# Performance work log

Hardware: AMD Instinct MI355X
Metric: run time of the kernel (lower is better)

Reference implementation:

```python
import jax, jax.numpy as jnp
import numpy as np

R_CUTOFF = 5.0
BASIS = 8
NMAX = 8
NSPECIES = 3
EMBED = 16


def _chebyshev_basis(r, r_cutoff, basis_size):
    fc = jnp.where(r < r_cutoff, 0.5 * jnp.cos(jnp.pi * r / r_cutoff) + 0.5, 0.0)
    x = 2.0 * (r / r_cutoff) ** 2 - 1.0
    polys = [jnp.ones_like(x), x]
    for n in range(2, basis_size):
        polys.append(2.0 * x * polys[-1] - polys[-2])
    basis = jnp.stack(polys[:basis_size], axis=-1)  # [E, basis]
    return 0.5 * (basis + 1.0) * fc[:, None]


def setup_inputs() -> dict:
    key = jax.random.key(0)
    ks = jax.random.split(key, 12)
    N, K = 20000, 32
    E = N * K
    positions = jax.random.normal(ks[0], (N, 3), dtype=jnp.float32)
    species = jax.random.randint(ks[1], (N,), 0, NSPECIES, dtype=jnp.int32)
    magmoms = jax.random.normal(ks[2], (N, 3), dtype=jnp.float32)
    # i-major edge list: exactly K edges per atom, grouped by center atom.
    i_idx = jnp.repeat(jnp.arange(N, dtype=jnp.int32), K)
    j_idx = jax.random.randint(ks[3], (E,), 0, N, dtype=jnp.int32)
    edge_index = jnp.stack([i_idx, j_idx], axis=0)
    shifts = jnp.zeros((E, 3), dtype=jnp.float32)
    rb_coefficients = 0.1 * jax.random.normal(ks[4], (NSPECIES * NSPECIES, NMAX, BASIS), dtype=jnp.float32)
    species_embedding = 0.1 * jax.random.normal(ks[5], (NSPECIES, EMBED), dtype=jnp.float32)
    struct_dim = NMAX + NMAX * (NMAX + 1)  # 80
    mag_dim = 3 + 7 * NMAX + 3 * NMAX * NMAX  # 251
    return {
        'positions': positions, 'species': species, 'magmoms': magmoms,
        'edge_index': edge_index, 'shifts': shifts,
        'rb_coefficients': rb_coefficients, 'species_embedding': species_embedding,
        'struct_shift': jnp.zeros(struct_dim, jnp.float32),
        'struct_scale': jnp.ones(struct_dim, jnp.float32),
        'mag_shift': jnp.zeros(mag_dim, jnp.float32),
        'mag_scale': jnp.ones(mag_dim, jnp.float32),
        'atomic_energy_shift': 0.1 * jax.random.normal(ks[6], (NSPECIES,), dtype=jnp.float32),
        'w_struct': 0.05 * jax.random.normal(ks[7], (EMBED + struct_dim,), dtype=jnp.float32),
        'b_struct': 0.05 * jax.random.normal(ks[8], (1,), dtype=jnp.float32),
        'w_mag': 0.05 * jax.random.normal(ks[9], (EMBED + mag_dim,), dtype=jnp.float32),
        'b_mag': 0.05 * jax.random.normal(ks[10], (1,), dtype=jnp.float32),
    }


def _forward(positions, magmoms, shifts, rb_coefficients, species_embedding,
             struct_shift, struct_scale, mag_shift, mag_scale, atomic_energy_shift,
             w_struct, b_struct, w_mag, b_mag, species, edge_index):
    N = positions.shape[0]
    E = edge_index.shape[1]
    K = E // N  # regular neighbor count (edge list is i-major)
    i_idx, j_idx = edge_index[0], edge_index[1]
    r_ij = positions[j_idx] - positions[i_idx] + shifts          # [E,3]
    dist = jnp.linalg.norm(r_ij, axis=-1)                        # [E]
    f_k = _chebyshev_basis(dist, R_CUTOFF, BASIS)                # [E,basis]
    pair_idx = species[i_idx] * NSPECIES + species[j_idx]
    phi = jnp.einsum('enk,ek->en', rb_coefficients[pair_idx], f_k)  # [E,n]
    seg = lambda x: jax.ops.segment_sum(x, i_idx, num_segments=N)
    d = jnp.maximum(dist, 1e-8)[:, None]
    r_hat = r_ij / d
    # --- structural descriptors ---
    d_radial = seg(phi)                                          # [N,n]
    P = seg(phi[:, :, None] * r_hat[:, None, :])                 # [N,n,3]
    PP = jnp.einsum('ina,ima->inm', P, P)
    tu = np.triu_indices(NMAX)
    d_ang_l1 = PP[:, tu[0], tu[1]]
    eye3 = jnp.eye(3, dtype=r_ij.dtype)
    traceless = r_hat[:, :, None] * r_hat[:, None, :] - eye3 / 3.0  # [E,3,3]
    Q = seg(phi[:, :, None, None] * traceless[:, None, :, :])       # [N,n,3,3]
    Qf = Q.reshape(N, NMAX, 9)
    QQ = jnp.einsum('ina,ima->inm', Qf, Qf)
    d_ang_l2 = QQ[:, tu[0], tu[1]]
    desc_struct = jnp.concatenate([d_radial, d_ang_l1, d_ang_l2], axis=-1)
    # --- magnetic descriptors ---
    u = jnp.sum(magmoms * magmoms, axis=-1)                      # [N]
    m_norm = jnp.linalg.norm(magmoms, axis=-1, keepdims=True)
    m_dir = jnp.where(m_norm > 1e-8, magmoms / jnp.maximum(m_norm, 1e-8), 0.0)
    M = seg(phi[:, :, None] * m_dir[j_idx][:, None, :])          # [N,n,3]
    # A_{nm}(i) = sum_{a<b within atom i's edge block} phi_n(a) phi_m(b) (r_a x r_b)
    phi_g = phi.reshape(N, K, NMAX)
    r_g = r_ij.reshape(N, K, 3)
    cross = jnp.cross(r_g[:, :, None, :], r_g[:, None, :, :])    # [N,K,K,3]
    mask = jnp.triu(jnp.ones((K, K), dtype=phi.dtype), k=1)
    tmp = jnp.einsum('iabd,ab,ibm->iamd', cross, mask, phi_g)    # [N,K,3,n]
    A = jnp.einsum('ian,iamd->inmd', phi_g, tmp)                 # [N,n,n,3]
    d_amp = jnp.stack([u, u ** 2, u ** 3], axis=-1)
    d_iso = jnp.sum(m_dir[:, None, :] * M, axis=-1)              # [N,n]
    Qm = jnp.einsum('anij,aj->ani', Q, m_dir)
    d_sia = jnp.sum(m_dir[:, None, :] * Qm, axis=-1)
    mQ = jnp.einsum('ai,amij->amj', m_dir, Q)
    d_sae = jnp.einsum('amj,anj->amn', mQ, M).reshape(N, -1)
    m_cross_M = jnp.cross(jnp.broadcast_to(m_dir[:, None, :], M.shape), M)
    d_dmi = jnp.einsum('inmd,imd->inm', A, m_cross_M).reshape(N, -1)
    u_col = u[:, None]
    d_amp_mix = jnp.concatenate([u_col * d_iso, u_col * d_sia, u_col * d_dmi], axis=-1)
    u_j = u[j_idx]
    d_nbr_amp = seg(phi * u_j[:, None])
    W = seg(phi[:, :, None] * (u_j[:, None] * m_dir[j_idx])[:, None, :])
    d_nbr_amp_ex = jnp.sum(m_dir[:, None, :] * W, axis=-1)
    d_nbr_amp_ex_mix = u_col * d_nbr_amp_ex
    desc_mag = jnp.concatenate([d_amp, d_iso, d_sia, d_sae, d_dmi, d_amp_mix,
                                d_nbr_amp, d_nbr_amp_ex, d_nbr_amp_ex_mix], axis=-1)
    # --- scaling + linear readout heads + per-species shift ---
    ds = (desc_struct - struct_shift) / struct_scale
    dm = (desc_mag - mag_shift) / mag_scale
    emb = species_embedding[species]
    e_struct = jnp.concatenate([emb, ds], axis=-1) @ w_struct + b_struct[0]
    e_mag = jnp.concatenate([emb, dm], axis=-1) @ w_mag + b_mag[0]
    return e_struct + e_mag + atomic_energy_shift[species]        # [N]


def reference(positions, species, magmoms, edge_index, shifts, rb_coefficients,
              species_embedding, struct_shift, struct_scale, mag_shift, mag_scale,
              atomic_energy_shift, w_struct, b_struct, w_mag, b_mag):
    return _forward(positions, magmoms, shifts, rb_coefficients, species_embedding,
                    struct_shift, struct_scale, mag_shift, mag_scale, atomic_energy_shift,
                    w_struct, b_struct, w_mag, b_mag, species, edge_index)
```

## Files before the change

kernel.cpp:

```cpp
#include <hip/hip_runtime.h>

#define NSPEC  3
#define EMBEDD 16
#define KMAX   32
#define RCUT   5.0f
#define PADR   36

__constant__ int TUN[36] = {0,0,0,0,0,0,0,0, 1,1,1,1,1,1,1, 2,2,2,2,2,2, 3,3,3,3,3, 4,4,4,4, 5,5,5, 6,6, 7};
__constant__ int TUM[36] = {0,1,2,3,4,5,6,7, 1,2,3,4,5,6,7, 2,3,4,5,6,7, 3,4,5,6,7, 4,5,6,7, 5,6,7, 6,7, 7};


struct __align__(16) AtomLds {
    float phiT[8 * PADR];
    float tT[8 * PADR];
    float rhx[KMAX], rhy[KMAX], rhz[KMAX];
    float mdx[KMAX], mdy[KMAX], mdz[KMAX];
    float uj[KMAX];
    float P[24], Q[48], M[24], W[24], mQ[24];
};

__global__ __launch_bounds__(256)
void magpot_setup(const float* __restrict__ sshift, const float* __restrict__ sscale,
                  const float* __restrict__ mshift, const float* __restrict__ mscale,
                  const float* __restrict__ wstruct, const float* __restrict__ bstruct,
                  const float* __restrict__ wmag, const float* __restrict__ bmag,
                  float* __restrict__ ws)
{
    __shared__ float red[4];
    const int t = threadIdx.x;
    float c = 0.0f;
    for (int idx = t; idx < 80; idx += 256) {
        const float w = wstruct[16 + idx] / sscale[idx];
        ws[idx] = w;
        c += w * sshift[idx];
    }
    for (int idx = t; idx < 251; idx += 256) {
        const float w = wmag[16 + idx] / mscale[idx];
        ws[80 + idx] = w;
        c += w * mshift[idx];
    }
    if (t < EMBEDD) ws[332 + t] = wstruct[t] + wmag[t];
    #pragma unroll
    for (int d = 1; d <= 32; d <<= 1) c += __shfl_xor(c, d, 64);
    if ((t & 63) == 0) red[t >> 6] = c;
    __syncthreads();
    if (t == 0) ws[331] = bstruct[0] + bmag[0] - (red[0] + red[1] + red[2] + red[3]);
}

__global__ __launch_bounds__(256, 5)
void magpot_main(const float* __restrict__ pos,
                 const int*   __restrict__ species,
                 const float* __restrict__ mag,
                 const int*   __restrict__ eidx,
                 const float* __restrict__ shifts,
                 const float* __restrict__ rb,
                 const float* __restrict__ semb,
                 const float* __restrict__ aes,
                 const float* __restrict__ ws,
                 float* __restrict__ out,
                 int N, int E, int K)
{
    __shared__ AtomLds lds[8];

    const int lane64 = threadIdx.x & 63;
    const int wv     = threadIdx.x >> 6;
    const int h      = lane64 >> 5;
    const int s      = lane64 & 31;
    const int i      = blockIdx.x * 8 + wv * 2 + h;
    const bool valid = (i < N);
    const int isafe  = valid ? i : 0;
    AtomLds& L = lds[wv * 2 + h];

    const float* wm = ws + 80;

    const float pix = pos[3*isafe+0], piy = pos[3*isafe+1], piz = pos[3*isafe+2];
    const int   spi = species[isafe];
    const float mgx = mag[3*isafe+0], mgy = mag[3*isafe+1], mgz = mag[3*isafe+2];
    const float u_i = mgx*mgx + mgy*mgy + mgz*mgz;
    const float mn_i = sqrtf(u_i);
    const float mi_inv = (mn_i > 1e-8f) ? (1.0f / mn_i) : 0.0f;
    const float mix = mgx*mi_inv, miy = mgy*mi_inv, miz = mgz*mi_inv;

    float phi[8];
    float rx = 0.0f, ry = 0.0f, rz = 0.0f;
    #pragma unroll
    for (int n = 0; n < 8; ++n) phi[n] = 0.0f;

    if (s < K) {
        const int e = isafe * K + s;
        const int j = eidx[E + e];
        rx = pos[3*j+0] - pix + shifts[3*e+0];
        ry = pos[3*j+1] - piy + shifts[3*e+1];
        rz = pos[3*j+2] - piz + shifts[3*e+2];
        const float dist = sqrtf(rx*rx + ry*ry + rz*rz);
        const float fc = (dist < RCUT)
            ? (0.5f * cosf(3.14159265358979323846f * dist * (1.0f/RCUT)) + 0.5f)
            : 0.0f;
        const float xr = dist * (1.0f/RCUT);
        const float x  = 2.0f * xr * xr - 1.0f;
        float f[8];
        {
            float Tm2 = 1.0f, Tm1 = x;
            f[0] = 0.5f * (Tm2 + 1.0f) * fc;
            f[1] = 0.5f * (Tm1 + 1.0f) * fc;
            #pragma unroll
            for (int k = 2; k < 8; ++k) {
                const float T = 2.0f * x * Tm1 - Tm2;
                Tm2 = Tm1; Tm1 = T;
                f[k] = 0.5f * (T + 1.0f) * fc;
            }
        }
        const int spj = species[j];
        const float4* rb4 = (const float4*)(rb + (spi * NSPEC + spj) * 64);
        #pragma unroll
        for (int n = 0; n < 8; ++n) {
            const float4 r0 = rb4[n*2+0];
            const float4 r1 = rb4[n*2+1];
            const float ph = r0.x*f[0] + r0.y*f[1] + r0.z*f[2] + r0.w*f[3]
                           + r1.x*f[4] + r1.y*f[5] + r1.z*f[6] + r1.w*f[7];
            phi[n] = ph;
            L.phiT[n*PADR + s] = ph;
        }
        const float dinv = 1.0f / fmaxf(dist, 1e-8f);
        L.rhx[s] = rx * dinv;
        L.rhy[s] = ry * dinv;
        L.rhz[s] = rz * dinv;
        const float mjx = mag[3*j+0], mjy = mag[3*j+1], mjz = mag[3*j+2];
        const float uj = mjx*mjx + mjy*mjy + mjz*mjz;
        const float mnj = sqrtf(uj);
        const float mjinv = (mnj > 1e-8f) ? (1.0f / mnj) : 0.0f;
        L.mdx[s] = mjx * mjinv;
        L.mdy[s] = mjy * mjinv;
        L.mdz[s] = mjz * mjinv;
        L.uj[s] = uj;
    } else {
        #pragma unroll
        for (int n = 0; n < 8; ++n) L.phiT[n*PADR + s] = 0.0f;
        L.rhx[s] = 0.0f; L.rhy[s] = 0.0f; L.rhz[s] = 0.0f;
        L.mdx[s] = 0.0f; L.mdy[s] = 0.0f; L.mdz[s] = 0.0f;
        L.uj[s] = 0.0f;
    }
    __syncthreads();

    float p = 0.0f;

    {
        const int k4 = s >> 3;
        const int n  = s & 7;
        const float4* phR = (const float4*)&L.phiT[n*PADR + k4*8];
        const float4* hxR = (const float4*)&L.rhx[k4*8];
        const float4* hyR = (const float4*)&L.rhy[k4*8];
        const float4* hzR = (const float4*)&L.rhz[k4*8];
        const float4* dxR = (const float4*)&L.mdx[k4*8];
        const float4* dyR = (const float4*)&L.mdy[k4*8];
        const float4* dzR = (const float4*)&L.mdz[k4*8];
        const float4* ujR = (const float4*)&L.uj[k4*8];

        float a_dr = 0.0f;
        float aP0 = 0.0f, aP1 = 0.0f, aP2 = 0.0f;
        float aQ0 = 0.0f, aQ1 = 0.0f, aQ2 = 0.0f, aQ3 = 0.0f, aQ4 = 0.0f, aQ5 = 0.0f;
        float aM0 = 0.0f, aM1 = 0.0f, aM2 = 0.0f;
        float a_nb = 0.0f;
        float aW0 = 0.0f, aW1 = 0.0f, aW2 = 0.0f;

        auto acc = [&](float ph, float hx, float hy, float hz,
                       float dx, float dy, float dz, float uj) {
            a_dr += ph;
            aP0 += ph*hx; aP1 += ph*hy; aP2 += ph*hz;
            aQ0 += ph*(hx*hx - (1.0f/3.0f));
            aQ1 += ph*(hx*hy);
            aQ2 += ph*(hx*hz);
            aQ3 += ph*(hy*hy - (1.0f/3.0f));
            aQ4 += ph*(hy*hz);
            aQ5 += ph*(hz*hz - (1.0f/3.0f));
            aM0 += ph*dx; aM1 += ph*dy; aM2 += ph*dz;
            const float pu = ph*uj;
            a_nb += pu;
            aW0 += pu*dx; aW1 += pu*dy; aW2 += pu*dz;
        };
        #pragma unroll
        for (int q = 0; q < 2; ++q) {
            const float4 ph4 = phR[q], hx4 = hxR[q], hy4 = hyR[q], hz4 = hzR[q];
            const float4 dx4 = dxR[q], dy4 = dyR[q], dz4 = dzR[q], uj4 = ujR[q];
            acc(ph4.x, hx4.x, hy4.x, hz4.x, dx4.x, dy4.x, dz4.x, uj4.x);
            acc(ph4.y, hx4.y, hy4.y, hz4.y, dx4.y, dy4.y, dz4.y, uj4.y);
            acc(ph4.z, hx4.z, hy4.z, hz4.z, dx4.z, dy4.z, dz4.z, uj4.z);
            acc(ph4.w, hx4.w, hy4.w, hz4.w, dx4.w, dy4.w, dz4.w, uj4.w);
        }
        #pragma unroll
        for (int d = 8; d <= 16; d <<= 1) {
            a_dr += __shfl_xor(a_dr, d, 64);
            aP0 += __shfl_xor(aP0, d, 64); aP1 += __shfl_xor(aP1, d, 64); aP2 += __shfl_xor(aP2, d, 64);
            aQ0 += __shfl_xor(aQ0, d, 64); aQ1 += __shfl_xor(aQ1, d, 64); aQ2 += __shfl_xor(aQ2, d, 64);
            aQ3 += __shfl_xor(aQ3, d, 64); aQ4 += __shfl_xor(aQ4, d, 64); aQ5 += __shfl_xor(aQ5, d, 64);
            aM0 += __shfl_xor(aM0, d, 64); aM1 += __shfl_xor(aM1, d, 64); aM2 += __shfl_xor(aM2, d, 64);
            a_nb += __shfl_xor(a_nb, d, 64);
            aW0 += __shfl_xor(aW0, d, 64); aW1 += __shfl_xor(aW1, d, 64); aW2 += __shfl_xor(aW2, d, 64);
        }
        if (k4 == 0) {
            L.P[n*3+0] = aP0; L.P[n*3+1] = aP1; L.P[n*3+2] = aP2;
            L.Q[n*6+0] = aQ0; L.Q[n*6+1] = aQ1; L.Q[n*6+2] = aQ2;
            L.Q[n*6+3] = aQ3; L.Q[n*6+4] = aQ4; L.Q[n*6+5] = aQ5;
            L.M[n*3+0] = aM0; L.M[n*3+1] = aM1; L.M[n*3+2] = aM2;
            L.W[n*3+0] = aW0; L.W[n*3+1] = aW1; L.W[n*3+2] = aW2;
            p += a_dr * ws[n];
            p += a_nb * wm[227 + n];
        }
        if (s == 8) {
            const float u2 = u_i * u_i;
            p += u_i * wm[0] + u2 * wm[1] + u2 * u_i * wm[2];
        }
        if (s < EMBEDD)
            p += semb[spi * EMBEDD + s] * ws[332 + s];
    }
    __syncthreads();

    {
        float S[8][3];
        #pragma unroll
        for (int m = 0; m < 8; ++m) {
            S[m][0] = phi[m] * rx;
            S[m][1] = phi[m] * ry;
            S[m][2] = phi[m] * rz;
        }
        #pragma unroll
        for (int d = 1; d <= 16; d <<= 1) {
            const bool ok = (s + d) < 32;
            #pragma unroll
            for (int m = 0; m < 8; ++m) {
                const float v0 = __shfl_down(S[m][0], d, 64);
                const float v1 = __shfl_down(S[m][1], d, 64);
                const float v2 = __shfl_down(S[m][2], d, 64);
                S[m][0] += ok ? v0 : 0.0f;
                S[m][1] += ok ? v1 : 0.0f;
                S[m][2] += ok ? v2 : 0.0f;
            }
        }
        #pragma unroll
        for (int m = 0; m < 8; ++m) {
            const float Sx = S[m][0] - phi[m]*rx;
            const float Sy = S[m][1] - phi[m]*ry;
            const float Sz = S[m][2] - phi[m]*rz;
            const float Mx = L.M[m*3+0], My = L.M[m*3+1], Mz = L.M[m*3+2];
            const float wx = miy*Mz - miz*My;
            const float wy = miz*Mx - mix*Mz;
            const float wz = mix*My - miy*Mx;
            const float cx = ry*Sz - rz*Sy;
            const float cy = rz*Sx - rx*Sz;
            const float cz = rx*Sy - ry*Sx;
            L.tT[m*PADR + s] = cx*wx + cy*wy + cz*wz;
        }
    }
    __syncthreads();

    {
        const int n  = s >> 2;
        const int mb = (s & 3) << 1;
        const float4* phR = (const float4*)&L.phiT[n*PADR];
        const float4* t0R = (const float4*)&L.tT[mb*PADR];
        const float4* t1R = (const float4*)&L.tT[(mb+1)*PADR];
        float d0 = 0.0f, d1 = 0.0f;
        #pragma unroll
        for (int q = 0; q < 8; ++q) {
            const float4 pv = phR[q];
            const float4 t0 = t0R[q];
            const float4 t1 = t1R[q];
            d0 += pv.x*t0.x + pv.y*t0.y + pv.z*t0.z + pv.w*t0.w;
            d1 += pv.x*t1.x + pv.y*t1.y + pv.z*t1.z + pv.w*t1.w;
        }
        const int i0 = n*8 + mb;
        p += d0 * wm[83 + i0]     + (u_i * d0) * wm[163 + i0];
        p += d1 * wm[83 + i0 + 1] + (u_i * d1) * wm[163 + i0 + 1];
    }

    if (s < 8) {
        const int n = s;
        const float Mx = L.M[n*3+0], My = L.M[n*3+1], Mz = L.M[n*3+2];
        const float diso = mix*Mx + miy*My + miz*Mz;
        const float q0 = L.Q[n*6+0], q1 = L.Q[n*6+1], q2 = L.Q[n*6+2];
        const float q3 = L.Q[n*6+3], q4 = L.Q[n*6+4], q5 = L.Q[n*6+5];
        const float dsia = q0*mix*mix + q3*miy*miy + q5*miz*miz
                         + 2.0f*(q1*mix*miy + q2*mix*miz + q4*miy*miz);
        L.mQ[n*3+0] = q0*mix + q1*miy + q2*miz;
        L.mQ[n*3+1] = q1*mix + q3*miy + q4*miz;
        L.mQ[n*3+2] = q2*mix + q4*miy + q5*miz;
        const float wx = L.W[n*3+0], wy = L.W[n*3+1], wz = L.W[n*3+2];
        const float dnex = mix*wx + miy*wy + miz*wz;
        p += diso * wm[3 + n]  + dsia * wm[11 + n]  + dnex * wm[235 + n]
           + u_i * (diso * wm[147 + n] + dsia * wm[155 + n] + dnex * wm[243 + n]);
    }
    __syncthreads();

    {
        #pragma unroll
        for (int t2 = 0; t2 < 2; ++t2) {
            const int idx = s + t2*32;
            const int m4 = idx >> 3, n4 = idx & 7;
            const float sae = L.mQ[m4*3+0]*L.M[n4*3+0]
                            + L.mQ[m4*3+1]*L.M[n4*3+1]
                            + L.mQ[m4*3+2]*L.M[n4*3+2];
            p += sae * wm[19 + idx];
        }
        #pragma unroll
        for (int t2 = 0; t2 < 2; ++t2) {
            const int idx = s + t2*32;
            if (idx < 36) {
                const int a = TUN[idx], b = TUM[idx];
                const float pp = L.P[a*3+0]*L.P[b*3+0] + L.P[a*3+1]*L.P[b*3+1] + L.P[a*3+2]*L.P[b*3+2];
                const float qq = L.Q[a*6+0]*L.Q[b*6+0] + L.Q[a*6+3]*L.Q[b*6+3] + L.Q[a*6+5]*L.Q[b*6+5]
                       + 2.0f*(L.Q[a*6+1]*L.Q[b*6+1] + L.Q[a*6+2]*L.Q[b*6+2] + L.Q[a*6+4]*L.Q[b*6+4]);
                p += pp * ws[8 + idx] + qq * ws[44 + idx];
            }
        }
    }

    #pragma unroll
    for (int d = 1; d <= 16; d <<= 1) p += __shfl_xor(p, d, 64);
    if (s == 0 && valid)
        out[i] = p + ws[331] + aes[spi];
}

extern "C" void kernel_launch(void* const* d_in, const int* in_sizes, int n_in,
                              void* d_out, int out_size, void* d_ws, size_t ws_size,
                              hipStream_t stream) {
    const float* pos     = (const float*)d_in[0];
    const int*   spc     = (const int*)  d_in[1];
    const float* mg      = (const float*)d_in[2];
    const int*   eidx    = (const int*)  d_in[3];
    const float* shf     = (const float*)d_in[4];
    const float* rb      = (const float*)d_in[5];
    const float* semb    = (const float*)d_in[6];
    const float* sshift  = (const float*)d_in[7];
    const float* sscale  = (const float*)d_in[8];
    const float* mshift  = (const float*)d_in[9];
    const float* mscale  = (const float*)d_in[10];
    const float* aes     = (const float*)d_in[11];
    const float* wstruct = (const float*)d_in[12];
    const float* bstruct = (const float*)d_in[13];
    const float* wmag    = (const float*)d_in[14];
    const float* bmag    = (const float*)d_in[15];
    float* out = (float*)d_out;
    float* ws  = (float*)d_ws;

    const int N = in_sizes[1];
    const int E = in_sizes[3] / 2;
    const int K = E / N;

    hipLaunchKernelGGL(magpot_setup, dim3(1), dim3(256), 0, stream,
                       sshift, sscale, mshift, mscale, wstruct, bstruct, wmag, bmag, ws);
    hipLaunchKernelGGL(magpot_main, dim3((N + 7) / 8), dim3(256), 0, stream,
                       pos, spc, mg, eidx, shf, rb, semb, aes, ws, out, N, E, K);
}
```

Before: 133.1 us.

## Replace shuffle-based scans and reductions with DPP and swizzle cross-lane ops

The lane-to-edge mapping is reversed (edge = 31 - lane) so that an inclusive prefix sum built from DPP row_shr and row_bcast yields the suffix sums the exclusive-scan step needs. This replaces the 24-value shfl_down scan that went through LDS. The k-reductions and the final per-atom reduction also move from __shfl_xor to DPP row_shr/row_bcast plus ds_swizzle. cosf is swapped for the hardware cos builtin, and the occupancy hint in launch bounds is dropped. The risks are DPP bound_ctrl/row_mask correctness across the 32-lane half-waves and the lower precision of the hardware cosine.

```diff
diff --git a/kernel.cpp b/kernel.cpp
--- a/kernel.cpp
+++ b/kernel.cpp
@@ -9,6 +9,36 @@
 __constant__ int TUN[36] = {0,0,0,0,0,0,0,0, 1,1,1,1,1,1,1, 2,2,2,2,2,2, 3,3,3,3,3, 4,4,4,4, 5,5,5, 6,6, 7};
 __constant__ int TUM[36] = {0,1,2,3,4,5,6,7, 1,2,3,4,5,6,7, 2,3,4,5,6,7, 3,4,5,6,7, 4,5,6,7, 5,6,7, 6,7, 7};
 
+
+template<int CTRL, int RMASK, bool BC>
+__device__ __forceinline__ float dpp_mov0(float x) {
+    return __int_as_float(__builtin_amdgcn_update_dpp(
+        0, __float_as_int(x), CTRL, RMASK, 0xF, BC));
+}
+__device__ __forceinline__ float prefix32(float x) {
+    x += dpp_mov0<0x111, 0xF, true >(x);
+    x += dpp_mov0<0x112, 0xF, true >(x);
+    x += dpp_mov0<0x114, 0xF, true >(x);
+    x += dpp_mov0<0x118, 0xF, true >(x);
+    x += dpp_mov0<0x142, 0xA, false>(x);
+    return x;
+}
+__device__ __forceinline__ float swz_xor16(float x) {
+    return __int_as_float(__builtin_amdgcn_ds_swizzle(__float_as_int(x), 0x401F));
+}
+__device__ __forceinline__ float red_k4(float x) {
+    x += dpp_mov0<0x128, 0xF, true>(x);
+    x += swz_xor16(x);
+    return x;
+}
+__device__ __forceinline__ float red32(float x) {
+    x += dpp_mov0<0x121, 0xF, true>(x);
+    x += dpp_mov0<0x122, 0xF, true>(x);
+    x += dpp_mov0<0x124, 0xF, true>(x);
+    x += dpp_mov0<0x128, 0xF, true>(x);
+    x += swz_xor16(x);
+    return x;
+}
 
 struct __align__(16) AtomLds {
     float phiT[8 * PADR];
@@ -47,7 +77,7 @@
     if (t == 0) ws[331] = bstruct[0] + bmag[0] - (red[0] + red[1] + red[2] + red[3]);
 }
 
-__global__ __launch_bounds__(256, 5)
+__global__ __launch_bounds__(256)
 void magpot_main(const float* __restrict__ pos,
                  const int*   __restrict__ species,
                  const float* __restrict__ mag,
@@ -66,6 +96,7 @@
     const int wv     = threadIdx.x >> 6;
     const int h      = lane64 >> 5;
     const int s      = lane64 & 31;
+    const int ea     = 31 - s;
     const int i      = blockIdx.x * 8 + wv * 2 + h;
     const bool valid = (i < N);
     const int isafe  = valid ? i : 0;
@@ -86,15 +117,15 @@
     #pragma unroll
     for (int n = 0; n < 8; ++n) phi[n] = 0.0f;
 
-    if (s < K) {
-        const int e = isafe * K + s;
+    if (ea < K) {
+        const int e = isafe * K + ea;
         const int j = eidx[E + e];
         rx = pos[3*j+0] - pix + shifts[3*e+0];
         ry = pos[3*j+1] - piy + shifts[3*e+1];
         rz = pos[3*j+2] - piz + shifts[3*e+2];
         const float dist = sqrtf(rx*rx + ry*ry + rz*rz);
         const float fc = (dist < RCUT)
-            ? (0.5f * cosf(3.14159265358979323846f * dist * (1.0f/RCUT)) + 0.5f)
+            ? (0.5f * __builtin_amdgcn_cosf(dist * 0.1f) + 0.5f)
             : 0.0f;
         const float xr = dist * (1.0f/RCUT);
         const float x  = 2.0f * xr * xr - 1.0f;
@@ -119,26 +150,26 @@
             const float ph = r0.x*f[0] + r0.y*f[1] + r0.z*f[2] + r0.w*f[3]
                            + r1.x*f[4] + r1.y*f[5] + r1.z*f[6] + r1.w*f[7];
             phi[n] = ph;
-            L.phiT[n*PADR + s] = ph;
+            L.phiT[n*PADR + ea] = ph;
         }
         const float dinv = 1.0f / fmaxf(dist, 1e-8f);
-        L.rhx[s] = rx * dinv;
-        L.rhy[s] = ry * dinv;
-        L.rhz[s] = rz * dinv;
+        L.rhx[ea] = rx * dinv;
+        L.rhy[ea] = ry * dinv;
+        L.rhz[ea] = rz * dinv;
         const float mjx = mag[3*j+0], mjy = mag[3*j+1], mjz = mag[3*j+2];
         const float uj = mjx*mjx + mjy*mjy + mjz*mjz;
         const float mnj = sqrtf(uj);
         const float mjinv = (mnj > 1e-8f) ? (1.0f / mnj) : 0.0f;
-        L.mdx[s] = mjx * mjinv;
-        L.mdy[s] = mjy * mjinv;
-        L.mdz[s] = mjz * mjinv;
-        L.uj[s] = uj;
+        L.mdx[ea] = mjx * mjinv;
+        L.mdy[ea] = mjy * mjinv;
+        L.mdz[ea] = mjz * mjinv;
+        L.uj[ea] = uj;
     } else {
         #pragma unroll
-        for (int n = 0; n < 8; ++n) L.phiT[n*PADR + s] = 0.0f;
-        L.rhx[s] = 0.0f; L.rhy[s] = 0.0f; L.rhz[s] = 0.0f;
-        L.mdx[s] = 0.0f; L.mdy[s] = 0.0f; L.mdz[s] = 0.0f;
-        L.uj[s] = 0.0f;
+        for (int n = 0; n < 8; ++n) L.phiT[n*PADR + ea] = 0.0f;
+        L.rhx[ea] = 0.0f; L.rhy[ea] = 0.0f; L.rhz[ea] = 0.0f;
+        L.mdx[ea] = 0.0f; L.mdy[ea] = 0.0f; L.mdz[ea] = 0.0f;
+        L.uj[ea] = 0.0f;
     }
     __syncthreads();
 
@@ -187,16 +218,14 @@
             acc(ph4.z, hx4.z, hy4.z, hz4.z, dx4.z, dy4.z, dz4.z, uj4.z);
             acc(ph4.w, hx4.w, hy4.w, hz4.w, dx4.w, dy4.w, dz4.w, uj4.w);
         }
-        #pragma unroll
-        for (int d = 8; d <= 16; d <<= 1) {
-            a_dr += __shfl_xor(a_dr, d, 64);
-            aP0 += __shfl_xor(aP0, d, 64); aP1 += __shfl_xor(aP1, d, 64); aP2 += __shfl_xor(aP2, d, 64);
-            aQ0 += __shfl_xor(aQ0, d, 64); aQ1 += __shfl_xor(aQ1, d, 64); aQ2 += __shfl_xor(aQ2, d, 64);
-            aQ3 += __shfl_xor(aQ3, d, 64); aQ4 += __shfl_xor(aQ4, d, 64); aQ5 += __shfl_xor(aQ5, d, 64);
-            aM0 += __shfl_xor(aM0, d, 64); aM1 += __shfl_xor(aM1, d, 64); aM2 += __shfl_xor(aM2, d, 64);
-            a_nb += __shfl_xor(a_nb, d, 64);
-            aW0 += __shfl_xor(aW0, d, 64); aW1 += __shfl_xor(aW1, d, 64); aW2 += __shfl_xor(aW2, d, 64);
-        }
+        a_dr = red_k4(a_dr);
+        aP0 = red_k4(aP0); aP1 = red_k4(aP1); aP2 = red_k4(aP2);
+        aQ0 = red_k4(aQ0); aQ1 = red_k4(aQ1); aQ2 = red_k4(aQ2);
+        aQ3 = red_k4(aQ3); aQ4 = red_k4(aQ4); aQ5 = red_k4(aQ5);
+        aM0 = red_k4(aM0); aM1 = red_k4(aM1); aM2 = red_k4(aM2);
+        a_nb = red_k4(a_nb);
+        aW0 = red_k4(aW0); aW1 = red_k4(aW1); aW2 = red_k4(aW2);
+
         if (k4 == 0) {
             L.P[n*3+0] = aP0; L.P[n*3+1] = aP1; L.P[n*3+2] = aP2;
             L.Q[n*6+0] = aQ0; L.Q[n*6+1] = aQ1; L.Q[n*6+2] = aQ2;
@@ -215,40 +244,30 @@
     }
     __syncthreads();
 
-    {
-        float S[8][3];
-        #pragma unroll
-        for (int m = 0; m < 8; ++m) {
-            S[m][0] = phi[m] * rx;
-            S[m][1] = phi[m] * ry;
-            S[m][2] = phi[m] * rz;
-        }
-        #pragma unroll
-        for (int d = 1; d <= 16; d <<= 1) {
-            const bool ok = (s + d) < 32;
-            #pragma unroll
-            for (int m = 0; m < 8; ++m) {
-                const float v0 = __shfl_down(S[m][0], d, 64);
-                const float v1 = __shfl_down(S[m][1], d, 64);
-                const float v2 = __shfl_down(S[m][2], d, 64);
-                S[m][0] += ok ? v0 : 0.0f;
-                S[m][1] += ok ? v1 : 0.0f;
-                S[m][2] += ok ? v2 : 0.0f;
-            }
-        }
-        #pragma unroll
-        for (int m = 0; m < 8; ++m) {
-            const float Sx = S[m][0] - phi[m]*rx;
-            const float Sy = S[m][1] - phi[m]*ry;
-            const float Sz = S[m][2] - phi[m]*rz;
+    #pragma unroll
+    for (int c = 0; c < 2; ++c) {
+        float wxv[4], wyv[4], wzv[4];
+        #pragma unroll
+        for (int mm = 0; mm < 4; ++mm) {
+            const int m = c*4 + mm;
             const float Mx = L.M[m*3+0], My = L.M[m*3+1], Mz = L.M[m*3+2];
-            const float wx = miy*Mz - miz*My;
-            const float wy = miz*Mx - mix*Mz;
-            const float wz = mix*My - miy*Mx;
+            wxv[mm] = miy*Mz - miz*My;
+            wyv[mm] = miz*Mx - mix*Mz;
+            wzv[mm] = mix*My - miy*Mx;
+        }
+        #pragma unroll
+        for (int mm = 0; mm < 4; ++mm) {
+            const int m = c*4 + mm;
+            const float vx = phi[m] * rx;
+            const float vy = phi[m] * ry;
+            const float vz = phi[m] * rz;
+            const float Sx = prefix32(vx) - vx;
+            const float Sy = prefix32(vy) - vy;
+            const float Sz = prefix32(vz) - vz;
             const float cx = ry*Sz - rz*Sy;
             const float cy = rz*Sx - rx*Sz;
             const float cz = rx*Sy - ry*Sx;
-            L.tT[m*PADR + s] = cx*wx + cy*wy + cz*wz;
+            L.tT[m*PADR + ea] = cx*wxv[mm] + cy*wyv[mm] + cz*wzv[mm];
         }
     }
     __syncthreads();
@@ -314,8 +333,7 @@
         }
     }
 
-    #pragma unroll
-    for (int d = 1; d <= 16; d <<= 1) p += __shfl_xor(p, d, 64);
+    p = red32(p);
     if (s == 0 && valid)
         out[i] = p + ws[331] + aes[spi];
 }
```

After: 122.1 us. -8.3%, faster.
